# Optimization experiments

Hardware: AMD Instinct MI355X
Metric: run time of the kernel (lower is better)

Reference implementation:

```python
import jax, jax.numpy as jnp
import numpy as np

EPS = 1e-5


def _conv(x, w, pad):
    return jax.lax.conv_general_dilated(
        x, w, (1, 1), [(pad, pad), (pad, pad)],
        dimension_numbers=('NCHW', 'OIHW', 'NCHW'))


def _reflect_pad1(x):
    return jnp.pad(x, ((0, 0), (0, 0), (1, 1), (1, 1)), mode='reflect')


def _instance_norm(x):
    m = x.mean((2, 3), keepdims=True)
    v = x.var((2, 3), keepdims=True)  # biased, as torch InstanceNorm2d
    return (x - m) * jax.lax.rsqrt(v + EPS)


def _batch_norm(x, g, b):
    m = x.mean((0, 2, 3), keepdims=True)
    v = x.var((0, 2, 3), keepdims=True)
    return (x - m) * jax.lax.rsqrt(v + EPS) * g.reshape(1, -1, 1, 1) + b.reshape(1, -1, 1, 1)


def _dct_ortho(x):
    # DCT-II with 'ortho' norm along last axis (same math as torch_dct.dct)
    N = x.shape[-1]
    v = jnp.concatenate([x[..., ::2], x[..., 1::2][..., ::-1]], axis=-1)
    Vc = jnp.fft.fft(v)
    k = jnp.arange(N) * (np.pi / (2.0 * N))
    V = Vc.real * jnp.cos(k) + Vc.imag * jnp.sin(k)
    scale = jnp.full((N,), 1.0 / np.sqrt(N / 2.0), dtype=x.dtype).at[0].set(1.0 / np.sqrt(float(N)))
    return V * scale


def _idct_ortho(X):
    # DCT-III (inverse of ortho DCT-II) along last axis (same math as torch_dct.idct)
    N = X.shape[-1]
    scale = jnp.full((N,), np.sqrt(N / 2.0), dtype=X.dtype).at[0].set(np.sqrt(float(N)))
    Xv = X * scale
    k = jnp.arange(N) * (np.pi / (2.0 * N))
    Wr, Wi = jnp.cos(k), jnp.sin(k)
    Vti = jnp.concatenate([jnp.zeros_like(Xv[..., :1]), -Xv[..., ::-1][..., :-1]], axis=-1)
    V = (Xv * Wr - Vti * Wi) + 1j * (Xv * Wi + Vti * Wr)
    v = jnp.fft.ifft(V).real
    out = jnp.zeros_like(v)
    out = out.at[..., ::2].set(v[..., : (N + 1) // 2])
    out = out.at[..., 1::2].set(v[..., ::-1][..., : N // 2])
    return out


def setup_inputs() -> dict:
    key = jax.random.key(0)
    ks = iter(jax.random.split(key, 32))
    B, C, H, W = 4, 128, 128, 128
    R = C // 16  # SFOM ratio
    d = {'x': jax.random.normal(next(ks), (B, C, H, W), jnp.float32)}
    d['conv1_w'] = jax.random.normal(next(ks), (C, C, 3, 3), jnp.float32) * 0.05
    d['conv1_b'] = jnp.zeros((C,), jnp.float32)
    d['conv2_w'] = jax.random.normal(next(ks), (C, C, 3, 3), jnp.float32) * 0.05
    d['conv2_b'] = jnp.zeros((C,), jnp.float32)
    # SFOM spectral attention MLP (torch Linear weights: [out, in])
    d['sa_w1'] = jax.random.normal(next(ks), (R, C), jnp.float32) * 0.1
    d['sa_w2'] = jax.random.normal(next(ks), (C, R), jnp.float32) * 0.1
    # SPEM dynamic-conv pyramid: 128->32->64->128->128->64->32, k=7
    chans = [(C, 32), (32, 64), (64, 128), (128, 128), (128, 64), (64, 32)]
    for i, (ci, co) in enumerate(chans, 1):
        d[f'dw{i}'] = jax.random.normal(next(ks), (co, ci, 7, 7), jnp.float32) * (0.05 / np.sqrt(ci))
        d[f'bg{i}'] = jnp.ones((co,), jnp.float32)
        d[f'bb{i}'] = jnp.zeros((co,), jnp.float32)
    d['spem_cw'] = jax.random.normal(next(ks), (1, 32, 1, 1), jnp.float32) * 0.1
    d['spem_cb'] = jnp.zeros((1,), jnp.float32)
    return d


def reference(x, conv1_w, conv1_b, conv2_w, conv2_b, sa_w1, sa_w2,
              dw1, bg1, bb1, dw2, bg2, bb2, dw3, bg3, bb3,
              dw4, bg4, bb4, dw5, bg5, bb5, dw6, bg6, bb6,
              spem_cw, spem_cb):
    # conv1: reflect pad 1 + conv(padding=1) -> spatial grows by 2
    out = _conv(_reflect_pad1(x), conv1_w, 1) + conv1_b.reshape(1, -1, 1, 1)
    out = jax.nn.relu(_instance_norm(out))
    out = _conv(_reflect_pad1(out), conv2_w, 1) + conv2_b.reshape(1, -1, 1, 1)
    out = _instance_norm(out)
    # SFOM channel attention via DCT gating
    B, C, H, W = out.shape
    dctx = _dct_ortho(out.reshape(B, C, H * W)).reshape(B, C, H, W)
    m = dctx.mean((2, 3))  # [B, C]
    gate = jax.nn.sigmoid(jax.nn.relu(m @ sa_w1.T) @ sa_w2.T)  # [B, C]
    idctx = _idct_ortho((dctx * gate[:, :, None, None]).reshape(B, C, H * W)).reshape(B, C, H, W)
    out = jax.nn.sigmoid((out + idctx) * 0.5) * out
    # SPEM spatial attention; DynamicConv2d repeats one shared filter per sample,
    # which is mathematically identical to a plain conv with that filter.
    h = out
    for w_, g_, b_ in ((dw1, bg1, bb1), (dw2, bg2, bb2), (dw3, bg3, bb3),
                       (dw4, bg4, bb4), (dw5, bg5, bb5), (dw6, bg6, bb6)):
        h = jax.nn.relu(_batch_norm(_conv(h, w_, 3), g_, b_))
    sa = jax.nn.sigmoid(_conv(h, spem_cw, 0) + spem_cb.reshape(1, -1, 1, 1))
    return sa * out
```

## Files before the change

### kernel.cpp

```cpp
#include <hip/hip_runtime.h>
#include <math.h>

#define B_    4
#define HW1   (130*130)
#define HW2   (132*132)
#define NBUF  ((size_t)B_*128*HW2)
#define EPS_  1e-5f
#define PI_   3.14159265358979f

typedef _Float16 half8 __attribute__((ext_vector_type(8)));
typedef _Float16 half4_ __attribute__((ext_vector_type(4)));
typedef float    float4_ __attribute__((ext_vector_type(4)));

struct WPackArgs {
  const float* src[8];
  _Float16*    dst[8];
  int cout[8], cin[8], kk[8];
  int off[9];
};
__global__ void wpack_all(WPackArgs p) {
  int idx = blockIdx.x * blockDim.x + threadIdx.x;
  if (idx >= p.off[8]) return;
  int s = 0;
  while (idx >= p.off[s + 1]) ++s;
  int i = idx - p.off[s];
  int Cin = p.cin[s], K = p.kk[s];
  int KK = K * K, COG = p.cout[s] / 16;
  int j    = i & 7;
  int lane = (i >> 3) & 63;
  int rest = i >> 9;
  int g    = rest % COG; rest /= COG;
  int tap  = rest % KK;
  int cc   = rest / KK;
  int n = lane & 15, q = lane >> 4;
  int co = g * 16 + n;
  int ci = cc * 32 + q * 8 + j;
  p.dst[s][i] = (_Float16)p.src[s][((size_t)co * Cin + ci) * KK + tap];
}

__global__ void to_nhwc(const float* __restrict__ in, _Float16* __restrict__ out,
                        int C, int HW) {
  __shared__ float t[32][65];
  int b = blockIdx.z, c0 = blockIdx.y * 32, p0 = blockIdx.x * 64;
  int tid = threadIdx.x;
  for (int i = 0; i < 8; ++i) {
    int e = i * 256 + tid; int cl = e >> 6, pl = e & 63;
    int p = p0 + pl;
    float v = 0.f;
    if (p < HW) v = in[((size_t)b * C + c0 + cl) * HW + p];
    t[cl][pl] = v;
  }
  __syncthreads();
  for (int i = 0; i < 8; ++i) {
    int e = i * 256 + tid; int pl = e >> 5, cl = e & 31;
    int p = p0 + pl;
    if (p < HW) out[((size_t)b * HW + p) * C + c0 + cl] = (_Float16)t[cl][pl];
  }
}

__global__ void zerok(float* p, int n) {
  int i = blockIdx.x * blockDim.x + threadIdx.x;
  if (i < n) p[i] = 0.f;
}

template<int CIN, int COUT, int K, int HIN, int HOUT, bool REFLECT, int AFF, bool RELU, bool POB>
__global__ __launch_bounds__(256, 2) void conv_mfma(
    const _Float16* __restrict__ act, const _Float16* __restrict__ wp,
    const float* __restrict__ sums_in, const float* __restrict__ gam,
    const float* __restrict__ bet, float invn, float* __restrict__ sums_out,
    _Float16* __restrict__ out) {
  constexpr int NWC = (COUT >= 64) ? 2 : 1;
  constexpr int WCO = COUT / NWC;
  constexpr int MR  = WCO / 16;
  constexpr int NWR = 4 / NWC;
  constexpr int ROWS = NWR * 4;
  constexpr int PADc = (K - 1) / 2;
  constexpr int IR = ROWS + K - 1;
  constexpr int XW = 16 + K - 1;
  constexpr int CH = IR * 4 * XW;
  constexpr int COG = COUT / 16;
  constexpr int KK = K * K;
  constexpr int XT = (HOUT + 15) / 16;

  __shared__ half8 smem[CH];
  __shared__ float2 snorm[CIN];
  __shared__ float bsum[COUT * 2];

  const int xt = blockIdx.x % XT, yt = blockIdx.x / XT;
  const int x0 = xt * 16, y0 = yt * ROWS;
  const int b = blockIdx.z;
  const int tid = threadIdx.x;
  const int lane = tid & 63, w = tid >> 6;
  const int wc = (NWC == 2) ? (w & 1) : 0;
  const int wr = (NWC == 2) ? (w >> 1) : w;
  const int n = lane & 15, q = lane >> 4;

  if (AFF) {
    if (tid < CIN) {
      int idx = (AFF == 1 ? b * CIN : 0) + tid;
      float m  = sums_in[idx * 2] * invn;
      float vr = sums_in[idx * 2 + 1] * invn - m * m;
      float sc = rsqrtf(vr + EPS_);
      if (AFF == 2) sc *= gam[tid];
      float sh = (AFF == 2 ? bet[tid] : 0.f) - m * sc;
      snorm[tid] = make_float2(sc, sh);
    }
  }
  if (tid < COUT) { bsum[tid * 2] = 0.f; bsum[tid * 2 + 1] = 0.f; }

  float4_ acc[MR][4];
#pragma unroll
  for (int mi = 0; mi < MR; ++mi)
#pragma unroll
    for (int ni = 0; ni < 4; ++ni)
#pragma unroll
      for (int j = 0; j < 4; ++j) acc[mi][ni][j] = 0.f;

  const _Float16* actb = act + (size_t)b * HIN * HIN * CIN;

  for (int cc = 0; cc < CIN / 32; ++cc) {
    __syncthreads();
    float nsc[8], nsh[8];
    if (AFF) {
      int cb2 = cc * 32 + (tid & 3) * 8;
#pragma unroll
      for (int j = 0; j < 8; ++j) { float2 t = snorm[cb2 + j]; nsc[j] = t.x; nsh[j] = t.y; }
    }
    for (int e = tid; e < CH; e += 256) {
      int qq = e & 3, rx = e >> 2;
      int row = rx / XW, lx = rx % XW;
      int ty = y0 + row - PADc;
      int tx = x0 + lx - PADc;
      bool ok; int iy, ix;
      if (REFLECT) {
        ok = (ty >= 0 && ty < HIN + 2 && tx >= 0 && tx < HIN + 2);
        iy = (ty == 0) ? 1 : (ty == HIN + 1 ? HIN - 2 : ty - 1);
        ix = (tx == 0) ? 1 : (tx == HIN + 1 ? HIN - 2 : tx - 1);
      } else {
        ok = (ty >= 0 && ty < HIN && tx >= 0 && tx < HIN);
        iy = ty; ix = tx;
      }
      half8 v;
#pragma unroll
      for (int j = 0; j < 8; ++j) v[j] = (_Float16)0.f;
      if (ok) {
        v = *(const half8*)(actb + ((size_t)iy * HIN + ix) * CIN + cc * 32 + qq * 8);
        if (AFF) {
#pragma unroll
          for (int j = 0; j < 8; ++j) {
            float f = (float)v[j] * nsc[j] + nsh[j];
            if (RELU) f = fmaxf(f, 0.f);
            v[j] = (_Float16)f;
          }
        }
      }
      smem[(row * 4 + qq) * XW + lx] = v;
    }
    __syncthreads();
    auto ldA = [&](int tap, half8* a) {
#pragma unroll
      for (int mi = 0; mi < MR; ++mi) {
        int g = wc * MR + mi;
        a[mi] = *(const half8*)(wp + (((size_t)(cc * KK + tap) * COG + g) * 64 + lane) * 8);
      }
    };
    auto ldB = [&](int tap, half8* c) {
      int ky = tap / K, kx = tap % K;
#pragma unroll
      for (int ni = 0; ni < 4; ++ni)
        c[ni] = smem[((wr * 4 + ni + ky) * 4 + q) * XW + n + kx];
    };
    auto domf = [&](half8* a, half8* c) {
#pragma unroll
      for (int mi = 0; mi < MR; ++mi)
#pragma unroll
        for (int ni = 0; ni < 4; ++ni)
          acc[mi][ni] = __builtin_amdgcn_mfma_f32_16x16x32_f16(a[mi], c[ni], acc[mi][ni], 0, 0, 0);
    };
    half8 a0[MR], a1[MR], c0[4], c1[4];
    ldA(0, a0); ldB(0, c0);
    for (int tap = 0; tap + 1 < KK; tap += 2) {
      ldA(tap + 1, a1); ldB(tap + 1, c1);
      domf(a0, c0);
      ldA(tap + 2, a0); ldB(tap + 2, c0);
      domf(a1, c1);
    }
    domf(a0, c0);
  }

  const bool xv = (x0 + n) < HOUT;
#pragma unroll
  for (int mi = 0; mi < MR; ++mi) {
#pragma unroll
    for (int j = 0; j < 4; ++j) {
      float s = 0.f, s2 = 0.f;
#pragma unroll
      for (int ni = 0; ni < 4; ++ni) {
        int y = y0 + wr * 4 + ni;
        float f = acc[mi][ni][j];
        bool v = xv && (y < HOUT);
        s  += v ? f : 0.f;
        s2 += v ? f * f : 0.f;
      }
#pragma unroll
      for (int off = 1; off < 16; off <<= 1) {
        s  += __shfl_xor(s,  off, 64);
        s2 += __shfl_xor(s2, off, 64);
      }
      if (n == 0) {
        int co = wc * WCO + mi * 16 + q * 4 + j;
        atomicAdd(&bsum[co * 2],     s);
        atomicAdd(&bsum[co * 2 + 1], s2);
      }
    }
  }
  _Float16* outb = out + (size_t)b * HOUT * HOUT * COUT;
#pragma unroll
  for (int mi = 0; mi < MR; ++mi) {
#pragma unroll
    for (int ni = 0; ni < 4; ++ni) {
      int y = y0 + wr * 4 + ni, x = x0 + n;
      if (y < HOUT && x < HOUT) {
        int co = wc * WCO + mi * 16 + q * 4;
        half4_ h;
#pragma unroll
        for (int j = 0; j < 4; ++j) h[j] = (_Float16)acc[mi][ni][j];
        *(half4_*)(outb + ((size_t)y * HOUT + x) * COUT + co) = h;
      }
    }
  }
  __syncthreads();
  if (tid < COUT) {
    int idx = (POB ? b * COUT : 0) + tid;
    atomicAdd(&sums_out[idx * 2],     bsum[tid * 2]);
    atomicAdd(&sums_out[idx * 2 + 1], bsum[tid * 2 + 1]);
  }
}

__global__ void wdctk(float* __restrict__ wd, int N) {
  int i = blockIdx.x * blockDim.x + threadIdx.x;
  if (i >= N) return;
  float Nf = (float)N;
  float c2 = 0.5f * sqrtf(2.f / Nf);
  float a  = sqrtf(1.f / Nf) - c2;
  float phi = PI_ / (4.f * Nf) * (2.f * i + 1.f);
  float cot = cosf(phi) / sinf(phi);
  wd[i] = a + ((i & 1) ? -c2 : c2) * cot;
}

__global__ void mdctk(const _Float16* __restrict__ x, const float* __restrict__ wd,
                      const float* __restrict__ sums2, float invn,
                      float* __restrict__ md, int HW) {
  int b = blockIdx.z, tid = threadIdx.x;
  int c = tid & 127, pr = tid >> 7;
  int slab = blockIdx.x, nsl = gridDim.x;
  float m  = sums2[(b * 128 + c) * 2] * invn;
  float sc = rsqrtf(sums2[(b * 128 + c) * 2 + 1] * invn - m * m + EPS_);
  float sh = -m * sc;
  const _Float16* xb = x + (size_t)b * HW * 128;
  float s = 0.f;
  for (int p = slab * 2 + pr; p < HW; p += nsl * 2)
    s += ((float)xb[(size_t)p * 128 + c] * sc + sh) * wd[p];
  __shared__ float l1[256];
  l1[tid] = s;
  __syncthreads();
  if (tid < 128) atomicAdd(&md[b * 128 + c], l1[tid] + l1[tid + 128]);
}

__global__ void gatek(const float* __restrict__ md, const float* __restrict__ w1,
                      const float* __restrict__ w2, float* __restrict__ gate) {
  __shared__ float t1[4][8];
  int tid = threadIdx.x;
  const float invN = 1.f / (float)HW2;
  if (tid < 32) {
    int b = tid >> 3, r = tid & 7;
    float s = 0.f;
    for (int c = 0; c < 128; ++c) s += md[b * 128 + c] * invN * w1[r * 128 + c];
    t1[b][r] = fmaxf(s, 0.f);
  }
  __syncthreads();
  int b = tid >> 7, c = tid & 127;
  float s = 0.f;
#pragma unroll
  for (int r = 0; r < 8; ++r) s += t1[b][r] * w2[c * 8 + r];
  gate[tid] = 1.f / (1.f + expf(-s));
}

__global__ void sfomk(const _Float16* __restrict__ x, const float* __restrict__ sums2,
                      float invn, const float* __restrict__ gate,
                      _Float16* __restrict__ o, int HW) {
  size_t idx = (size_t)blockIdx.x * blockDim.x + threadIdx.x;
  size_t tot = (size_t)4 * HW * 16;
  if (idx >= tot) return;
  int cg = (int)(idx % 16);
  size_t bp = idx / 16;
  int b = (int)(bp / HW);
  half8 v = *(const half8*)(x + bp * 128 + cg * 8);
  half8 r;
#pragma unroll
  for (int j = 0; j < 8; ++j) {
    int c = cg * 8 + j;
    float m  = sums2[(b * 128 + c) * 2] * invn;
    float sc = rsqrtf(sums2[(b * 128 + c) * 2 + 1] * invn - m * m + EPS_);
    float f = (float)v[j] * sc - m * sc;
    float g = gate[b * 128 + c];
    float s = 1.f / (1.f + expf(-(f * (1.f + g) * 0.5f)));
    r[j] = (_Float16)(s * f);
  }
  *(half8*)(o + bp * 128 + cg * 8) = r;
}

__global__ void sak(const _Float16* __restrict__ h, const float* __restrict__ sums6,
                    float invn, const float* __restrict__ gam, const float* __restrict__ bet,
                    const float* __restrict__ cw, const float* __restrict__ cb,
                    float* __restrict__ sa) {
  __shared__ float ssc[32], ssh[32];
  int tid = threadIdx.x;
  if (tid < 32) {
    float m  = sums6[tid * 2] * invn;
    float sc = rsqrtf(sums6[tid * 2 + 1] * invn - m * m + EPS_) * gam[tid];
    ssc[tid] = sc;
    ssh[tid] = bet[tid] - m * sc;
  }
  __syncthreads();
  int idx = blockIdx.x * blockDim.x + tid;
  if (idx >= 4 * HW2) return;
  const _Float16* p = h + (size_t)idx * 32;
  float s = cb[0];
#pragma unroll
  for (int c = 0; c < 32; ++c)
    s += fmaxf((float)p[c] * ssc[c] + ssh[c], 0.f) * cw[c];
  sa[idx] = 1.f / (1.f + expf(-s));
}

__global__ void finalt(const _Float16* __restrict__ o, const float* __restrict__ sa,
                       float* __restrict__ out) {
  __shared__ float t[32][65];
  int b = blockIdx.z, c0 = blockIdx.y * 32, p0 = blockIdx.x * 64;
  int tid = threadIdx.x;
  for (int i = 0; i < 8; ++i) {
    int e = i * 256 + tid; int pl = e >> 5, cl = e & 31;
    int p = p0 + pl;
    if (p < HW2)
      t[cl][pl] = (float)o[((size_t)b * HW2 + p) * 128 + c0 + cl] * sa[b * HW2 + p];
  }
  __syncthreads();
  for (int i = 0; i < 8; ++i) {
    int e = i * 256 + tid; int cl = e >> 6, pl = e & 63;
    int p = p0 + pl;
    if (p < HW2)
      out[((size_t)b * 128 + c0 + cl) * HW2 + p] = t[cl][pl];
  }
}

extern "C" void kernel_launch(void* const* d_in, const int* in_sizes, int n_in,
                              void* d_out, int out_size, void* d_ws, size_t ws_size,
                              hipStream_t stream) {
  const float* x     = (const float*)d_in[0];
  const float* c1w   = (const float*)d_in[1];
  const float* c2w   = (const float*)d_in[3];
  const float* sa_w1 = (const float*)d_in[5];
  const float* sa_w2 = (const float*)d_in[6];
  const float* dw[6] = {(const float*)d_in[7],  (const float*)d_in[10], (const float*)d_in[13],
                        (const float*)d_in[16], (const float*)d_in[19], (const float*)d_in[22]};
  const float* bg[6] = {(const float*)d_in[8],  (const float*)d_in[11], (const float*)d_in[14],
                        (const float*)d_in[17], (const float*)d_in[20], (const float*)d_in[23]};
  const float* bb[6] = {(const float*)d_in[9],  (const float*)d_in[12], (const float*)d_in[15],
                        (const float*)d_in[18], (const float*)d_in[21], (const float*)d_in[24]};
  const float* cw    = (const float*)d_in[25];
  const float* cb    = (const float*)d_in[26];
  float* out = (float*)d_out;

  char* wsp = (char*)d_ws;
  auto alloc = [&](size_t bytes) { char* p = wsp; wsp += (bytes + 255) & ~(size_t)255; return p; };
  _Float16* B0 = (_Float16*)alloc(NBUF * 2);
  _Float16* B1 = (_Float16*)alloc(NBUF * 2);
  _Float16* B2 = (_Float16*)alloc(NBUF * 2);
  _Float16* B3 = (_Float16*)alloc(NBUF * 2);
  _Float16* wp_c1 = (_Float16*)alloc((size_t)128 * 128 * 9 * 2);
  _Float16* wp_c2 = (_Float16*)alloc((size_t)128 * 128 * 9 * 2);
  const int sci[6] = {128, 32, 64, 128, 128, 64};
  const int sco[6] = {32, 64, 128, 128, 64, 32};
  _Float16* wp_d[6];
  for (int i = 0; i < 6; ++i) wp_d[i] = (_Float16*)alloc((size_t)sco[i] * sci[i] * 49 * 2);
  float* SUMS = (float*)alloc(8704 * 4);
  float* s_c1 = SUMS;
  float* s_c2 = SUMS + 1024;
  float* s_l[6];
  for (int i = 0; i < 6; ++i) s_l[i] = SUMS + 2048 + i * 1024;
  float* md   = SUMS + 8192;
  float* gate = (float*)alloc(512 * 4);
  float* wd   = (float*)alloc((size_t)HW2 * 4);
  float* sa   = (float*)alloc((size_t)4 * HW2 * 4);

  {
    WPackArgs p;
    p.src[0] = c1w; p.dst[0] = wp_c1; p.cout[0] = 128; p.cin[0] = 128; p.kk[0] = 3;
    p.src[1] = c2w; p.dst[1] = wp_c2; p.cout[1] = 128; p.cin[1] = 128; p.kk[1] = 3;
    for (int i = 0; i < 6; ++i) {
      p.src[2 + i] = dw[i]; p.dst[2 + i] = wp_d[i];
      p.cout[2 + i] = sco[i]; p.cin[2 + i] = sci[i]; p.kk[2 + i] = 7;
    }
    p.off[0] = 0;
    for (int i = 0; i < 8; ++i) p.off[i + 1] = p.off[i] + p.cout[i] * p.cin[i] * p.kk[i] * p.kk[i];
    wpack_all<<<(p.off[8] + 255) / 256, 256, 0, stream>>>(p);
  }

  to_nhwc<<<dim3(16384 / 64, 4, 4), 256, 0, stream>>>(x, B0, 128, 16384);
  zerok<<<34, 256, 0, stream>>>(SUMS, 8704);

  const float i1 = 1.f / (float)HW1, i2 = 1.f / (float)HW2, ib = 1.f / (4.f * HW2);

  conv_mfma<128, 128, 3, 128, 130, true, 0, false, true><<<dim3(9 * 17, 1, 4), 256, 0, stream>>>(
      B0, wp_c1, nullptr, nullptr, nullptr, 0.f, s_c1, B1);
  conv_mfma<128, 128, 3, 130, 132, true, 1, true, true><<<dim3(9 * 17, 1, 4), 256, 0, stream>>>(
      B1, wp_c2, s_c1, nullptr, nullptr, i1, s_c2, B2);

  wdctk<<<(HW2 + 255) / 256, 256, 0, stream>>>(wd, HW2);
  mdctk<<<dim3(128, 1, 4), 256, 0, stream>>>(B2, wd, s_c2, i2, md, HW2);
  gatek<<<1, 512, 0, stream>>>(md, sa_w1, sa_w2, gate);
  { size_t tot = (size_t)4 * HW2 * 16;
    sfomk<<<(int)((tot + 255) / 256), 256, 0, stream>>>(B2, s_c2, i2, gate, B3, HW2); }

  conv_mfma<128, 32, 7, 132, 132, false, 0, false, false><<<dim3(9 * 9, 1, 4), 256, 0, stream>>>(
      B3, wp_d[0], nullptr, nullptr, nullptr, 0.f, s_l[0], B0);
  conv_mfma<32, 64, 7, 132, 132, false, 2, true, false><<<dim3(9 * 17, 1, 4), 256, 0, stream>>>(
      B0, wp_d[1], s_l[0], bg[0], bb[0], ib, s_l[1], B1);
  conv_mfma<64, 128, 7, 132, 132, false, 2, true, false><<<dim3(9 * 17, 1, 4), 256, 0, stream>>>(
      B1, wp_d[2], s_l[1], bg[1], bb[1], ib, s_l[2], B0);
  conv_mfma<128, 128, 7, 132, 132, false, 2, true, false><<<dim3(9 * 17, 1, 4), 256, 0, stream>>>(
      B0, wp_d[3], s_l[2], bg[2], bb[2], ib, s_l[3], B1);
  conv_mfma<128, 64, 7, 132, 132, false, 2, true, false><<<dim3(9 * 17, 1, 4), 256, 0, stream>>>(
      B1, wp_d[4], s_l[3], bg[3], bb[3], ib, s_l[4], B0);
  conv_mfma<64, 32, 7, 132, 132, false, 2, true, false><<<dim3(9 * 9, 1, 4), 256, 0, stream>>>(
      B0, wp_d[5], s_l[4], bg[4], bb[4], ib, s_l[5], B1);

  sak<<<(4 * HW2 + 255) / 256, 256, 0, stream>>>(B1, s_l[5], ib, bg[5], bb[5], cw, cb, sa);
  finalt<<<dim3((HW2 + 63) / 64, 4, 4), 256, 0, stream>>>(B3, sa, out);
}
```

Baseline: 740.9 us.

## Double-buffer conv input slabs in LDS with register-staged prefetch

Replaces the single shared-memory input tile with two buffers. The global loads for the next 32-channel slab are issued into registers before the MFMA loop and written to the other buffer afterwards, so load latency overlaps compute and one barrier per slab goes away. Gather offsets and reflect indices are also computed once instead of every slab. In exchange, LDS use doubles and more registers are live, which may lower occupancy under launch_bounds(256,2). The manual lgkmcnt wait plus raw s_barrier also has to order LDS writes correctly.

```diff
diff --git a/kernel.cpp b/kernel.cpp
--- a/kernel.cpp
+++ b/kernel.cpp
@@ -81,8 +81,10 @@
   constexpr int COG = COUT / 16;
   constexpr int KK = K * K;
   constexpr int XT = (HOUT + 15) / 16;
-
-  __shared__ half8 smem[CH];
+  constexpr int NSLAB = CIN / 32;
+  constexpr int NST = (CH + 255) / 256;
+
+  __shared__ half8 smem[2][CH];
   __shared__ float2 snorm[CIN];
   __shared__ float bsum[COUT * 2];
 
@@ -118,15 +120,13 @@
 
   const _Float16* actb = act + (size_t)b * HIN * HIN * CIN;
 
-  for (int cc = 0; cc < CIN / 32; ++cc) {
-    __syncthreads();
-    float nsc[8], nsh[8];
-    if (AFF) {
-      int cb2 = cc * 32 + (tid & 3) * 8;
-#pragma unroll
-      for (int j = 0; j < 8; ++j) { float2 t = snorm[cb2 + j]; nsc[j] = t.x; nsh[j] = t.y; }
-    }
-    for (int e = tid; e < CH; e += 256) {
+  int sidx[NST];
+  int soff[NST];
+#pragma unroll
+  for (int i = 0; i < NST; ++i) {
+    int e = tid + i * 256;
+    sidx[i] = -1; soff[i] = -1;
+    if (e < CH) {
       int qq = e & 3, rx = e >> 2;
       int row = rx / XW, lx = rx % XW;
       int ty = y0 + row - PADc;
@@ -140,23 +140,54 @@
         ok = (ty >= 0 && ty < HIN && tx >= 0 && tx < HIN);
         iy = ty; ix = tx;
       }
-      half8 v;
-#pragma unroll
-      for (int j = 0; j < 8; ++j) v[j] = (_Float16)0.f;
-      if (ok) {
-        v = *(const half8*)(actb + ((size_t)iy * HIN + ix) * CIN + cc * 32 + qq * 8);
-        if (AFF) {
+      sidx[i] = (row * 4 + qq) * XW + lx;
+      if (ok) soff[i] = (iy * HIN + ix) * CIN + qq * 8;
+    }
+  }
+
+  auto ldS = [&](int cc, half8* v) {
+#pragma unroll
+    for (int i = 0; i < NST; ++i) {
+#pragma unroll
+      for (int j = 0; j < 8; ++j) v[i][j] = (_Float16)0.f;
+      if (soff[i] >= 0) v[i] = *(const half8*)(actb + soff[i] + cc * 32);
+    }
+  };
+  auto wrS = [&](int cc, int buf, half8* v) {
+    float nsc[8], nsh[8];
+    if (AFF) {
+      int cb2 = cc * 32 + (tid & 3) * 8;
+#pragma unroll
+      for (int j = 0; j < 8; ++j) { float2 t = snorm[cb2 + j]; nsc[j] = t.x; nsh[j] = t.y; }
+    }
+#pragma unroll
+    for (int i = 0; i < NST; ++i) {
+      if (sidx[i] >= 0) {
+        half8 t = v[i];
+        if (AFF && soff[i] >= 0) {
 #pragma unroll
           for (int j = 0; j < 8; ++j) {
-            float f = (float)v[j] * nsc[j] + nsh[j];
+            float f = (float)t[j] * nsc[j] + nsh[j];
             if (RELU) f = fmaxf(f, 0.f);
-            v[j] = (_Float16)f;
+            t[j] = (_Float16)f;
           }
         }
-      }
-      smem[(row * 4 + qq) * XW + lx] = v;
-    }
-    __syncthreads();
+        smem[buf][sidx[i]] = t;
+      }
+    }
+  };
+
+  half8 stg[NST];
+  ldS(0, stg);
+  __syncthreads();
+  wrS(0, 0, stg);
+
+  for (int cc = 0; cc < NSLAB; ++cc) {
+    const int cur = cc & 1;
+    if (cc + 1 < NSLAB) ldS(cc + 1, stg);
+    asm volatile("s_waitcnt lgkmcnt(0)" ::: "memory");
+    __builtin_amdgcn_s_barrier();
+
     auto ldA = [&](int tap, half8* a) {
 #pragma unroll
       for (int mi = 0; mi < MR; ++mi) {
@@ -168,7 +199,7 @@
       int ky = tap / K, kx = tap % K;
 #pragma unroll
       for (int ni = 0; ni < 4; ++ni)
-        c[ni] = smem[((wr * 4 + ni + ky) * 4 + q) * XW + n + kx];
+        c[ni] = smem[cur][((wr * 4 + ni + ky) * 4 + q) * XW + n + kx];
     };
     auto domf = [&](half8* a, half8* c) {
 #pragma unroll
@@ -186,6 +217,8 @@
       domf(a1, c1);
     }
     domf(a0, c0);
+
+    if (cc + 1 < NSLAB) wrS(cc + 1, cur ^ 1, stg);
   }
 
   const bool xv = (x0 + n) < HOUT;
```

After: 736.6 us (median of 2 runs). Within noise of the previous version (-0.6%).
